# Kernel tuning notes

Measured on AMD Instinct MI355X. Metric: run time of the kernel, lower is better.

Reference implementation:

```python
import jax, jax.numpy as jnp
import numpy as np

B, S, E, H, V, O = 64, 512, 128, 1024, 128, 128


def setup_inputs() -> dict:
    key = jax.random.key(0)
    ks = jax.random.split(key, 16)
    nrm = lambda k, shp, s=0.05: s * jax.random.normal(k, shp, dtype=jnp.float32)
    return {
        "inputs": jax.random.randint(ks[0], (B, S), 0, V),
        "carry": jnp.zeros((B, H), dtype=jnp.float32),
        "embedding": nrm(ks[1], (V, E), 0.1),
        # GRUCell params (flax convention: input denses 'ir','iz','in' have bias;
        # hidden denses 'hr','hz' no bias; 'hn' has bias)
        "Wir": nrm(ks[2], (E, H)), "bir": jnp.zeros((H,), jnp.float32),
        "Whr": nrm(ks[3], (H, H)),
        "Wiz": nrm(ks[4], (E, H)), "biz": jnp.zeros((H,), jnp.float32),
        "Whz": nrm(ks[5], (H, H)),
        "Win": nrm(ks[6], (E, H)), "bin_": jnp.zeros((H,), jnp.float32),
        "Whn": nrm(ks[7], (H, H)), "bhn": jnp.zeros((H,), jnp.float32),
        "Wh": nrm(ks[8], (H, H)), "bh": jnp.zeros((H,), jnp.float32),
        "Wo": nrm(ks[9], (H, O)), "bo": jnp.zeros((O,), jnp.float32),
    }


def reference(inputs, carry, embedding, Wir, bir, Whr, Wiz, biz, Whz,
              Win, bin_, Whn, bhn, Wh, bh, Wo, bo):
    # Embedding lookup: [B, S, E]
    embed = jnp.take(embedding, inputs, axis=0)

    # GRU scan over time (axis=1 of embed)
    def step(h, x):  # h: [B,H], x: [B,E]
        r = jax.nn.sigmoid(x @ Wir + bir + h @ Whr)
        z = jax.nn.sigmoid(x @ Wiz + biz + h @ Whz)
        n = jnp.tanh(x @ Win + bin_ + r * (h @ Whn + bhn))
        h_new = (1.0 - z) * n + z * h
        return h_new, h_new

    xs = jnp.swapaxes(embed, 0, 1)  # [S, B, E]
    carry_out, ys = jax.lax.scan(step, carry, xs)  # ys: [S, B, H]
    outputs = jnp.swapaxes(ys, 0, 1).reshape(-1, H)  # [B*S, H]

    hidden = outputs @ Wh + bh            # Dense hidden_size
    logits = hidden @ Wo + bo             # Dense output_size -> [B*S, O]
    return (carry_out, logits)
```

## Files before the change

### kernel.cpp

```cpp
#include <hip/hip_runtime.h>
#include <hip/hip_cooperative_groups.h>
#include <math.h>

namespace cg = cooperative_groups;

#define Bp 64
#define Sp 512
#define Ep 128
#define Hp 1024
#define Vp 128
#define Op 128
#define BH (Bp * Hp)

typedef short s8v __attribute__((ext_vector_type(8)));
typedef float f4v __attribute__((ext_vector_type(4)));

#define WS_XV    0
#define WS_WHI   (WS_XV + Vp*3*Hp)
#define WS_WLO   (WS_WHI + (3*Hp*Hp)/2)
#define WS_YSH   (WS_WLO + (3*Hp*Hp)/2)
#define WS_HLOP  (WS_YSH + ((size_t)(Sp+1)*BH)/2)
#define WS_WHBH  (WS_HLOP + (2*BH)/2)
#define WS_WHBL  (WS_WHBH + (Hp*Hp)/2)
#define WS_WOBH  (WS_WHBL + (Hp*Hp)/2)
#define WS_WOBL  (WS_WOBH + (Op*Hp)/2)
#define WS_BAR   (WS_WOBL + (Op*Hp)/2)
#define WS_FLOATS (WS_BAR + 4*256)

__device__ __forceinline__ unsigned short f2bf(float x) {
  union { float f; unsigned u; } v; v.f = x;
  unsigned r = v.u + 0x7fffu + ((v.u >> 16) & 1u);
  return (unsigned short)(r >> 16);
}
__device__ __forceinline__ float bf2f(unsigned short h) {
  union { unsigned u; float f; } v; v.u = ((unsigned)h) << 16;
  return v.f;
}

__device__ __forceinline__ s8v ald16(const unsigned short* p) {
  union { unsigned long long q[2]; s8v v; } u;
  const unsigned long long* qp = (const unsigned long long*)p;
  u.q[0] = __hip_atomic_load(qp,     __ATOMIC_RELAXED, __HIP_MEMORY_SCOPE_AGENT);
  u.q[1] = __hip_atomic_load(qp + 1, __ATOMIC_RELAXED, __HIP_MEMORY_SCOPE_AGENT);
  return u.v;
}
__device__ __forceinline__ void ast8(unsigned short* p, unsigned long long v) {
  __hip_atomic_store((unsigned long long*)p, v, __ATOMIC_RELAXED, __HIP_MEMORY_SCOPE_AGENT);
}

__global__ __launch_bounds__(256) void xv_kernel(
    const float* __restrict__ emb,
    const float* __restrict__ Wir, const float* __restrict__ bir,
    const float* __restrict__ Wiz, const float* __restrict__ biz,
    const float* __restrict__ Win, const float* __restrict__ bin_,
    float* __restrict__ XV) {
  int n = blockIdx.x * 256 + threadIdx.x;
  int v = blockIdx.y;
  int g = n >> 10;
  int j = n & (Hp - 1);
  const float* W = (g == 0) ? Wir : ((g == 1) ? Wiz : Win);
  const float* bias = (g == 0) ? bir : ((g == 1) ? biz : bin_);
  float acc = bias[j];
  const float* ev = emb + (size_t)v * Ep;
  for (int e = 0; e < Ep; ++e) acc += ev[e] * W[(size_t)e * Hp + j];
  XV[(size_t)v * (3 * Hp) + n] = acc;
}

__global__ void wpack_kernel(const float* __restrict__ Whr,
                             const float* __restrict__ Whz,
                             const float* __restrict__ Whn,
                             unsigned short* __restrict__ Whi,
                             unsigned short* __restrict__ Wlo) {
  __shared__ float tile[32][33];
  int g = blockIdx.z;
  const float* src = (g == 0) ? Whr : ((g == 1) ? Whz : Whn);
  int kb = blockIdx.x * 32;
  int jb32 = blockIdx.y * 32;
  int tx = threadIdx.x, ty = threadIdx.y;
  #pragma unroll
  for (int i = 0; i < 4; ++i)
    tile[ty + 8 * i][tx] = src[(size_t)(kb + ty + 8 * i) * Hp + (jb32 + tx)];
  __syncthreads();
  #pragma unroll
  for (int i = 0; i < 4; ++i) {
    int jl = ty + 8 * i;
    int j = jb32 + jl;
    int dstRow = ((j >> 4) * 3 + g) * 16 + (j & 15);
    float w = tile[tx][jl];
    unsigned short hi = f2bf(w);
    Whi[(size_t)dstRow * Hp + kb + tx] = hi;
    Wlo[(size_t)dstRow * Hp + kb + tx] = f2bf(w - bf2f(hi));
  }
}

__global__ void tsplit_kernel(const float* __restrict__ src, int K, int N,
                              unsigned short* __restrict__ dhi,
                              unsigned short* __restrict__ dlo) {
  __shared__ float tile[32][33];
  int kb = blockIdx.x * 32, nb = blockIdx.y * 32;
  int tx = threadIdx.x, ty = threadIdx.y;
  #pragma unroll
  for (int i = 0; i < 4; ++i)
    tile[ty + 8 * i][tx] = src[(size_t)(kb + ty + 8 * i) * N + nb + tx];
  __syncthreads();
  #pragma unroll
  for (int i = 0; i < 4; ++i) {
    int nl = ty + 8 * i;
    float w = tile[tx][nl];
    unsigned short hi = f2bf(w);
    dhi[(size_t)(nb + nl) * K + kb + tx] = hi;
    dlo[(size_t)(nb + nl) * K + kb + tx] = f2bf(w - bf2f(hi));
  }
}

__global__ void h0_kernel(const float* __restrict__ carry,
                          unsigned short* __restrict__ ysH,
                          unsigned short* __restrict__ hloP,
                          unsigned* __restrict__ bar) {
  int i = blockIdx.x * 256 + threadIdx.x;
  float h = carry[i];
  unsigned short hi = f2bf(h);
  ysH[i] = hi;
  hloP[i] = f2bf(h - bf2f(hi));
  if (i < 4 * 256) bar[i] = 0u;
}

__global__ __launch_bounds__(256, 1) void gru_scan(
    const float* __restrict__ carry,
    unsigned short* ysH,
    const unsigned short* __restrict__ Whi,
    const unsigned short* __restrict__ Wlo,
    const float* __restrict__ XV,
    const int* __restrict__ toks,
    const float* __restrict__ bhn,
    unsigned short* hloP,
    unsigned* bar) {
  __shared__ float part[3 * 4 * 64 * 4];
  __shared__ unsigned short hst[2][16][16];

  const int tid = threadIdx.x;
  const int wv = tid >> 6, lane = tid & 63;
  const int mb = blockIdx.x >> 6, jb = blockIdx.x & 63;
  const int col = lane & 15, kq = lane >> 4;

  unsigned* ctr = bar + mb * 256;

  const int kbase = wv * 256 + kq * 8;
  const unsigned short* bhp[3];
  const unsigned short* blp[3];
  #pragma unroll
  for (int g = 0; g < 3; ++g) {
    const size_t rowoff = ((size_t)(jb * 3 + g) * 16 + col) * Hp + kbase;
    bhp[g] = Whi + rowoff;
    blp[g] = Wlo + rowoff;
  }

  const int erow = tid >> 4, ecol = tid & 15;
  const int eb = mb * 16 + erow;
  const int ej = jb * 16 + ecol;
  const int elane = (erow >> 2) * 16 + ecol;
  const int er = erow & 3;
  const float bhnv = bhn[ej];

  const size_t aBase = (size_t)(mb * 16 + col) * Hp + kbase;
  const size_t eOff = (size_t)eb * Hp + ej;

  float holdR = carry[eOff];
  int tok0 = toks[eb * Sp + 0];
  const float* xvp0 = XV + (size_t)tok0 * (3 * Hp) + ej;
  float xr = xvp0[0], xz = xvp0[Hp], xn = xvp0[2 * Hp];

  const int splane = tid >> 6;
  const int srow = (tid >> 2) & 15;
  const int squad = tid & 3;
  const size_t sOff = (size_t)(mb * 16 + srow) * Hp + jb * 16 + squad * 4;

  for (int t = 0; t < Sp; ++t) {
    const unsigned short* hhiR = ysH + (size_t)t * BH;
    const unsigned short* hloR = hloP + (size_t)(t & 1) * BH;
    unsigned short* hhiW = ysH + (size_t)(t + 1) * BH;
    unsigned short* hloW = hloP + (size_t)((t + 1) & 1) * BH;

    s8v ah[8], al[8];
    #pragma unroll
    for (int c = 0; c < 8; ++c) {
      ah[c] = ald16(hhiR + aBase + (size_t)c * 32);
      al[c] = ald16(hloR + aBase + (size_t)c * 32);
    }

    float xrN, xzN, xnN;
    {
      int tN = (t + 1 < Sp) ? (t + 1) : t;
      int tokN = toks[eb * Sp + tN];
      const float* xvpN = XV + (size_t)tokN * (3 * Hp) + ej;
      xrN = xvpN[0];
      xzN = xvpN[Hp];
      xnN = xvpN[2 * Hp];
    }

    f4v ar = {0.f, 0.f, 0.f, 0.f}, az = {0.f, 0.f, 0.f, 0.f}, an = {0.f, 0.f, 0.f, 0.f};
    #pragma unroll
    for (int c = 0; c < 8; ++c) {
      s8v b0 = *(const s8v*)(bhp[0] + c * 32);
      s8v b1 = *(const s8v*)(bhp[1] + c * 32);
      s8v b2 = *(const s8v*)(bhp[2] + c * 32);
      s8v l0 = *(const s8v*)(blp[0] + c * 32);
      s8v l1 = *(const s8v*)(blp[1] + c * 32);
      s8v l2 = *(const s8v*)(blp[2] + c * 32);
      ar = __builtin_amdgcn_mfma_f32_16x16x32_bf16(ah[c], b0, ar, 0, 0, 0);
      az = __builtin_amdgcn_mfma_f32_16x16x32_bf16(ah[c], b1, az, 0, 0, 0);
      an = __builtin_amdgcn_mfma_f32_16x16x32_bf16(ah[c], b2, an, 0, 0, 0);
      ar = __builtin_amdgcn_mfma_f32_16x16x32_bf16(al[c], b0, ar, 0, 0, 0);
      az = __builtin_amdgcn_mfma_f32_16x16x32_bf16(al[c], b1, az, 0, 0, 0);
      an = __builtin_amdgcn_mfma_f32_16x16x32_bf16(al[c], b2, an, 0, 0, 0);
      ar = __builtin_amdgcn_mfma_f32_16x16x32_bf16(ah[c], l0, ar, 0, 0, 0);
      az = __builtin_amdgcn_mfma_f32_16x16x32_bf16(ah[c], l1, az, 0, 0, 0);
      an = __builtin_amdgcn_mfma_f32_16x16x32_bf16(ah[c], l2, an, 0, 0, 0);
    }

    *(f4v*)&part[((0 * 4 + wv) * 64 + lane) * 4] = ar;
    *(f4v*)&part[((1 * 4 + wv) * 64 + lane) * 4] = az;
    *(f4v*)&part[((2 * 4 + wv) * 64 + lane) * 4] = an;
    __syncthreads();

    float sr = 0.f, sz = 0.f, sn = 0.f;
    #pragma unroll
    for (int w = 0; w < 4; ++w) {
      sr += part[((0 * 4 + w) * 64 + elane) * 4 + er];
      sz += part[((1 * 4 + w) * 64 + elane) * 4 + er];
      sn += part[((2 * 4 + w) * 64 + elane) * 4 + er];
    }

    float rg = 1.f / (1.f + expf(-(sr + xr)));
    float zg = 1.f / (1.f + expf(-(sz + xz)));
    float ng = tanhf(xn + rg * (sn + bhnv));
    float hnew = (1.f - zg) * ng + zg * holdR;

    unsigned short hi16 = f2bf(hnew);
    hst[0][erow][ecol] = hi16;
    hst[1][erow][ecol] = f2bf(hnew - bf2f(hi16));

    holdR = hnew;
    xr = xrN; xz = xzN; xn = xnN;

    __syncthreads();
    if (tid < 128) {
      unsigned long long v = *(const unsigned long long*)&hst[splane][srow][squad * 4];
      ast8((splane ? hloW : hhiW) + sOff, v);
    }

    __threadfence_block();
    __syncthreads();
    if (tid == 0) {
      __hip_atomic_fetch_add(ctr, 1u, __ATOMIC_RELAXED, __HIP_MEMORY_SCOPE_AGENT);
      unsigned target = 64u * (unsigned)(t + 1);
      while (__hip_atomic_load(ctr, __ATOMIC_RELAXED, __HIP_MEMORY_SCOPE_AGENT) < target)
        __builtin_amdgcn_s_sleep(2);
    }
    __syncthreads();
  }
}

__global__ __launch_bounds__(256, 1) void dense_kernel(
    const unsigned short* __restrict__ ysH,
    const unsigned short* __restrict__ WhbH, const unsigned short* __restrict__ WhbL,
    const float* __restrict__ bh,
    const unsigned short* __restrict__ WobH, const unsigned short* __restrict__ WobL,
    const float* __restrict__ bo,
    float* __restrict__ out) {
  __shared__ unsigned short aHi[32 * 16 * 4 * 8];
  __shared__ unsigned short hidBf[32 * 16 * 4 * 8];

  const int tid = threadIdx.x;
  const int wv = tid >> 6, lane = tid & 63;
  const int col = lane & 15, kq = lane >> 4;
  const int r0 = blockIdx.x * 16;
  const int bq = r0 / Sp, s0 = r0 % Sp;

  for (int i = tid; i < 16 * 128; i += 256) {
    int m = i >> 7, c8 = i & 127;
    int kc = c8 >> 2, kqi = c8 & 3;
    const uint4* src = (const uint4*)(ysH + ((size_t)(s0 + m + 1) * Bp + bq) * Hp) + c8;
    *(uint4*)&aHi[((kc * 16 + m) * 4 + kqi) * 8] = *src;
  }
  __syncthreads();

  f4v acc[16];
  #pragma unroll
  for (int nt = 0; nt < 16; ++nt) acc[nt] = (f4v){0.f, 0.f, 0.f, 0.f};
  for (int kc = 0; kc < 32; ++kc) {
    s8v a = *(const s8v*)&aHi[(kc * 64 + col * 4 + kq) * 8];
    const size_t koff = (size_t)kc * 32 + kq * 8;
    #pragma unroll
    for (int nt = 0; nt < 16; ++nt) {
      int n = wv * 256 + nt * 16 + col;
      s8v bHi = *(const s8v*)(WhbH + (size_t)n * Hp + koff);
      s8v bLo = *(const s8v*)(WhbL + (size_t)n * Hp + koff);
      acc[nt] = __builtin_amdgcn_mfma_f32_16x16x32_bf16(a, bHi, acc[nt], 0, 0, 0);
      acc[nt] = __builtin_amdgcn_mfma_f32_16x16x32_bf16(a, bLo, acc[nt], 0, 0, 0);
    }
  }
  #pragma unroll
  for (int nt = 0; nt < 16; ++nt) {
    int n = wv * 256 + nt * 16 + col;
    float bias = bh[n];
    int kc = n >> 5, kqi = (n >> 3) & 3, ii = n & 7;
    #pragma unroll
    for (int r = 0; r < 4; ++r) {
      int m = kq * 4 + r;
      hidBf[((kc * 16 + m) * 4 + kqi) * 8 + ii] = f2bf(acc[nt][r] + bias);
    }
  }
  __syncthreads();

  f4v lacc[2];
  lacc[0] = (f4v){0.f, 0.f, 0.f, 0.f};
  lacc[1] = (f4v){0.f, 0.f, 0.f, 0.f};
  for (int kc = 0; kc < 32; ++kc) {
    s8v a = *(const s8v*)&hidBf[(kc * 64 + col * 4 + kq) * 8];
    const size_t koff = (size_t)kc * 32 + kq * 8;
    #pragma unroll
    for (int ot = 0; ot < 2; ++ot) {
      int o = (wv * 2 + ot) * 16 + col;
      s8v bHi = *(const s8v*)(WobH + (size_t)o * Hp + koff);
      s8v bLo = *(const s8v*)(WobL + (size_t)o * Hp + koff);
      lacc[ot] = __builtin_amdgcn_mfma_f32_16x16x32_bf16(a, bHi, lacc[ot], 0, 0, 0);
      lacc[ot] = __builtin_amdgcn_mfma_f32_16x16x32_bf16(a, bLo, lacc[ot], 0, 0, 0);
    }
  }
  float* lo = out + (size_t)Bp * Hp;
  #pragma unroll
  for (int ot = 0; ot < 2; ++ot) {
    int o = (wv * 2 + ot) * 16 + col;
    float bias = bo[o];
    #pragma unroll
    for (int r = 0; r < 4; ++r) {
      int m = kq * 4 + r;
      lo[(size_t)(r0 + m) * Op + o] = lacc[ot][r] + bias;
    }
  }
}

__global__ void carry_kernel(const unsigned short* __restrict__ ysH,
                             const unsigned short* __restrict__ hloP,
                             float* __restrict__ out) {
  int i = blockIdx.x * 256 + threadIdx.x;
  out[i] = bf2f(ysH[(size_t)Sp * BH + i]) + bf2f(hloP[(size_t)(Sp & 1) * BH + i]);
}

extern "C" void kernel_launch(void* const* d_in, const int* in_sizes, int n_in,
                              void* d_out, int out_size, void* d_ws, size_t ws_size,
                              hipStream_t stream) {
  const int*   toks = (const int*)  d_in[0];
  const float* carry= (const float*)d_in[1];
  const float* emb  = (const float*)d_in[2];
  const float* Wir  = (const float*)d_in[3];
  const float* bir  = (const float*)d_in[4];
  const float* Whr  = (const float*)d_in[5];
  const float* Wiz  = (const float*)d_in[6];
  const float* biz  = (const float*)d_in[7];
  const float* Whz  = (const float*)d_in[8];
  const float* Win  = (const float*)d_in[9];
  const float* bin_ = (const float*)d_in[10];
  const float* Whn  = (const float*)d_in[11];
  const float* bhn  = (const float*)d_in[12];
  const float* Wh   = (const float*)d_in[13];
  const float* bh   = (const float*)d_in[14];
  const float* Wo   = (const float*)d_in[15];
  const float* bo   = (const float*)d_in[16];
  float* out = (float*)d_out;

  if (ws_size < WS_FLOATS * sizeof(float)) return;

  float* ws = (float*)d_ws;
  float* XV = ws + WS_XV;
  unsigned short* WhiP = (unsigned short*)(ws + WS_WHI);
  unsigned short* WloP = (unsigned short*)(ws + WS_WLO);
  unsigned short* ysH  = (unsigned short*)(ws + WS_YSH);
  unsigned short* hloP = (unsigned short*)(ws + WS_HLOP);
  unsigned short* WhbH = (unsigned short*)(ws + WS_WHBH);
  unsigned short* WhbL = (unsigned short*)(ws + WS_WHBL);
  unsigned short* WobH = (unsigned short*)(ws + WS_WOBH);
  unsigned short* WobL = (unsigned short*)(ws + WS_WOBL);
  unsigned* bar = (unsigned*)(ws + WS_BAR);

  xv_kernel<<<dim3(12, Vp), 256, 0, stream>>>(emb, Wir, bir, Wiz, biz, Win, bin_, XV);
  wpack_kernel<<<dim3(Hp / 32, Hp / 32, 3), dim3(32, 8), 0, stream>>>(Whr, Whz, Whn, WhiP, WloP);
  tsplit_kernel<<<dim3(Hp / 32, Hp / 32), dim3(32, 8), 0, stream>>>(Wh, Hp, Hp, WhbH, WhbL);
  tsplit_kernel<<<dim3(Hp / 32, Op / 32), dim3(32, 8), 0, stream>>>(Wo, Hp, Op, WobH, WobL);
  h0_kernel<<<BH / 256, 256, 0, stream>>>(carry, ysH, hloP, bar);

  {
    void* args[] = {(void*)&carry, (void*)&ysH, (void*)&WhiP, (void*)&WloP,
                    (void*)&XV, (void*)&toks, (void*)&bhn,
                    (void*)&hloP, (void*)&bar};
    hipLaunchCooperativeKernel((const void*)gru_scan, dim3(256), dim3(256),
                               args, 0, stream);
  }

  carry_kernel<<<BH / 256, 256, 0, stream>>>(ysH, hloP, out);
  dense_kernel<<<(Bp * Sp) / 16, 256, 0, stream>>>(ysH, WhbH, WhbL, bh, WobH, WobL, bo, out);
}
```

Baseline: 4.516 ms.

## Replace per-group counter barrier with per-block flags and two batch groups per block

The scan kernel now launches 128 blocks instead of 256. Each block handles one hidden-column tile for two batch groups in turn. The atomic counter barrier that every block spun on is replaced by per-(batch group, column block) step flags, so a block waits only until the 64 producers of the group it is about to read have published. The goal is to cut barrier latency and let one group's compute overlap with the other group's wait. The cost is that each block does twice the sequential MFMA work per step and there is half as much parallelism.

```diff
diff --git a/kernel.cpp b/kernel.cpp
--- a/kernel.cpp
+++ b/kernel.cpp
@@ -24,8 +24,8 @@
 #define WS_WHBL  (WS_WHBH + (Hp*Hp)/2)
 #define WS_WOBH  (WS_WHBL + (Hp*Hp)/2)
 #define WS_WOBL  (WS_WOBH + (Op*Hp)/2)
-#define WS_BAR   (WS_WOBL + (Op*Hp)/2)
-#define WS_FLOATS (WS_BAR + 4*256)
+#define WS_FLG   (WS_WOBL + (Op*Hp)/2)
+#define WS_FLOATS (WS_FLG + 1024)
 
 __device__ __forceinline__ unsigned short f2bf(float x) {
   union { float f; unsigned u; } v; v.f = x;
@@ -116,13 +116,13 @@
 __global__ void h0_kernel(const float* __restrict__ carry,
                           unsigned short* __restrict__ ysH,
                           unsigned short* __restrict__ hloP,
-                          unsigned* __restrict__ bar) {
+                          unsigned* __restrict__ flg) {
   int i = blockIdx.x * 256 + threadIdx.x;
   float h = carry[i];
   unsigned short hi = f2bf(h);
   ysH[i] = hi;
   hloP[i] = f2bf(h - bf2f(hi));
-  if (i < 4 * 256) bar[i] = 0u;
+  if (i < 1024) flg[i] = 0u;
 }
 
 __global__ __launch_bounds__(256, 1) void gru_scan(
@@ -134,16 +134,14 @@
     const int* __restrict__ toks,
     const float* __restrict__ bhn,
     unsigned short* hloP,
-    unsigned* bar) {
+    unsigned* flg) {
   __shared__ float part[3 * 4 * 64 * 4];
   __shared__ unsigned short hst[2][16][16];
 
   const int tid = threadIdx.x;
   const int wv = tid >> 6, lane = tid & 63;
-  const int mb = blockIdx.x >> 6, jb = blockIdx.x & 63;
+  const int jb = blockIdx.x >> 1, mp = blockIdx.x & 1;
   const int col = lane & 15, kq = lane >> 4;
-
-  unsigned* ctr = bar + mb * 256;
 
   const int kbase = wv * 256 + kq * 8;
   const unsigned short* bhp[3];
@@ -156,24 +154,32 @@
   }
 
   const int erow = tid >> 4, ecol = tid & 15;
-  const int eb = mb * 16 + erow;
   const int ej = jb * 16 + ecol;
   const int elane = (erow >> 2) * 16 + ecol;
   const int er = erow & 3;
   const float bhnv = bhn[ej];
 
-  const size_t aBase = (size_t)(mb * 16 + col) * Hp + kbase;
-  const size_t eOff = (size_t)eb * Hp + ej;
-
-  float holdR = carry[eOff];
-  int tok0 = toks[eb * Sp + 0];
-  const float* xvp0 = XV + (size_t)tok0 * (3 * Hp) + ej;
-  float xr = xvp0[0], xz = xvp0[Hp], xn = xvp0[2 * Hp];
-
   const int splane = tid >> 6;
   const int srow = (tid >> 2) & 15;
   const int squad = tid & 3;
-  const size_t sOff = (size_t)(mb * 16 + srow) * Hp + jb * 16 + squad * 4;
+
+  int mbA[2];
+  int ebA[2];
+  size_t aBase[2], eOff[2], sOff[2];
+  float holdR[2], xr[2], xz[2], xn[2];
+  #pragma unroll
+  for (int i = 0; i < 2; ++i) {
+    int mb = 2 * mp + i;
+    mbA[i] = mb;
+    ebA[i] = mb * 16 + erow;
+    aBase[i] = (size_t)(mb * 16 + col) * Hp + kbase;
+    eOff[i] = (size_t)ebA[i] * Hp + ej;
+    sOff[i] = (size_t)(mb * 16 + srow) * Hp + jb * 16 + squad * 4;
+    holdR[i] = carry[eOff[i]];
+    int tok0 = toks[ebA[i] * Sp + 0];
+    const float* xvp0 = XV + (size_t)tok0 * (3 * Hp) + ej;
+    xr[i] = xvp0[0]; xz[i] = xvp0[Hp]; xn[i] = xvp0[2 * Hp];
+  }
 
   for (int t = 0; t < Sp; ++t) {
     const unsigned short* hhiR = ysH + (size_t)t * BH;
@@ -181,83 +187,92 @@
     unsigned short* hhiW = ysH + (size_t)(t + 1) * BH;
     unsigned short* hloW = hloP + (size_t)((t + 1) & 1) * BH;
 
-    s8v ah[8], al[8];
-    #pragma unroll
-    for (int c = 0; c < 8; ++c) {
-      ah[c] = ald16(hhiR + aBase + (size_t)c * 32);
-      al[c] = ald16(hloR + aBase + (size_t)c * 32);
+    for (int i = 0; i < 2; ++i) {
+      const int mb = mbA[i];
+
+      if (t > 0) {
+        const unsigned* fp = flg + mb * 64 + lane;
+        while (true) {
+          unsigned f = __hip_atomic_load(fp, __ATOMIC_RELAXED, __HIP_MEMORY_SCOPE_AGENT);
+          if (__all((int)(f >= (unsigned)t))) break;
+          __builtin_amdgcn_s_sleep(1);
+        }
+      }
+
+      s8v ah[8], al[8];
+      #pragma unroll
+      for (int c = 0; c < 8; ++c) {
+        ah[c] = ald16(hhiR + aBase[i] + (size_t)c * 32);
+        al[c] = ald16(hloR + aBase[i] + (size_t)c * 32);
+      }
+
+      float xrN, xzN, xnN;
+      {
+        int tN = (t + 1 < Sp) ? (t + 1) : t;
+        int tokN = toks[ebA[i] * Sp + tN];
+        const float* xvpN = XV + (size_t)tokN * (3 * Hp) + ej;
+        xrN = xvpN[0];
+        xzN = xvpN[Hp];
+        xnN = xvpN[2 * Hp];
+      }
+
+      f4v ar = {0.f, 0.f, 0.f, 0.f}, az = {0.f, 0.f, 0.f, 0.f}, an = {0.f, 0.f, 0.f, 0.f};
+      #pragma unroll
+      for (int c = 0; c < 8; ++c) {
+        s8v b0 = *(const s8v*)(bhp[0] + c * 32);
+        s8v b1 = *(const s8v*)(bhp[1] + c * 32);
+        s8v b2 = *(const s8v*)(bhp[2] + c * 32);
+        s8v l0 = *(const s8v*)(blp[0] + c * 32);
+        s8v l1 = *(const s8v*)(blp[1] + c * 32);
+        s8v l2 = *(const s8v*)(blp[2] + c * 32);
+        ar = __builtin_amdgcn_mfma_f32_16x16x32_bf16(ah[c], b0, ar, 0, 0, 0);
+        az = __builtin_amdgcn_mfma_f32_16x16x32_bf16(ah[c], b1, az, 0, 0, 0);
+        an = __builtin_amdgcn_mfma_f32_16x16x32_bf16(ah[c], b2, an, 0, 0, 0);
+        ar = __builtin_amdgcn_mfma_f32_16x16x32_bf16(al[c], b0, ar, 0, 0, 0);
+        az = __builtin_amdgcn_mfma_f32_16x16x32_bf16(al[c], b1, az, 0, 0, 0);
+        an = __builtin_amdgcn_mfma_f32_16x16x32_bf16(al[c], b2, an, 0, 0, 0);
+        ar = __builtin_amdgcn_mfma_f32_16x16x32_bf16(ah[c], l0, ar, 0, 0, 0);
+        az = __builtin_amdgcn_mfma_f32_16x16x32_bf16(ah[c], l1, az, 0, 0, 0);
+        an = __builtin_amdgcn_mfma_f32_16x16x32_bf16(ah[c], l2, an, 0, 0, 0);
+      }
+
+      *(f4v*)&part[((0 * 4 + wv) * 64 + lane) * 4] = ar;
+      *(f4v*)&part[((1 * 4 + wv) * 64 + lane) * 4] = az;
+      *(f4v*)&part[((2 * 4 + wv) * 64 + lane) * 4] = an;
+      __syncthreads();
+
+      float sr = 0.f, sz = 0.f, sn = 0.f;
+      #pragma unroll
+      for (int w = 0; w < 4; ++w) {
+        sr += part[((0 * 4 + w) * 64 + elane) * 4 + er];
+        sz += part[((1 * 4 + w) * 64 + elane) * 4 + er];
+        sn += part[((2 * 4 + w) * 64 + elane) * 4 + er];
+      }
+
+      float rg = 1.f / (1.f + expf(-(sr + xr[i])));
+      float zg = 1.f / (1.f + expf(-(sz + xz[i])));
+      float ng = tanhf(xn[i] + rg * (sn + bhnv));
+      float hnew = (1.f - zg) * ng + zg * holdR[i];
+
+      unsigned short hi16 = f2bf(hnew);
+      hst[0][erow][ecol] = hi16;
+      hst[1][erow][ecol] = f2bf(hnew - bf2f(hi16));
+
+      holdR[i] = hnew;
+      xr[i] = xrN; xz[i] = xzN; xn[i] = xnN;
+
+      __syncthreads();
+      if (tid < 128) {
+        unsigned long long v = *(const unsigned long long*)&hst[splane][srow][squad * 4];
+        ast8((splane ? hloW : hhiW) + sOff[i], v);
+      }
+
+      __threadfence_block();
+      __syncthreads();
+      if (tid == 0)
+        __hip_atomic_store(flg + mb * 64 + jb, (unsigned)(t + 1),
+                           __ATOMIC_RELAXED, __HIP_MEMORY_SCOPE_AGENT);
     }
-
-    float xrN, xzN, xnN;
-    {
-      int tN = (t + 1 < Sp) ? (t + 1) : t;
-      int tokN = toks[eb * Sp + tN];
-      const float* xvpN = XV + (size_t)tokN * (3 * Hp) + ej;
-      xrN = xvpN[0];
-      xzN = xvpN[Hp];
-      xnN = xvpN[2 * Hp];
-    }
-
-    f4v ar = {0.f, 0.f, 0.f, 0.f}, az = {0.f, 0.f, 0.f, 0.f}, an = {0.f, 0.f, 0.f, 0.f};
-    #pragma unroll
-    for (int c = 0; c < 8; ++c) {
-      s8v b0 = *(const s8v*)(bhp[0] + c * 32);
-      s8v b1 = *(const s8v*)(bhp[1] + c * 32);
-      s8v b2 = *(const s8v*)(bhp[2] + c * 32);
-      s8v l0 = *(const s8v*)(blp[0] + c * 32);
-      s8v l1 = *(const s8v*)(blp[1] + c * 32);
-      s8v l2 = *(const s8v*)(blp[2] + c * 32);
-      ar = __builtin_amdgcn_mfma_f32_16x16x32_bf16(ah[c], b0, ar, 0, 0, 0);
-      az = __builtin_amdgcn_mfma_f32_16x16x32_bf16(ah[c], b1, az, 0, 0, 0);
-      an = __builtin_amdgcn_mfma_f32_16x16x32_bf16(ah[c], b2, an, 0, 0, 0);
-      ar = __builtin_amdgcn_mfma_f32_16x16x32_bf16(al[c], b0, ar, 0, 0, 0);
-      az = __builtin_amdgcn_mfma_f32_16x16x32_bf16(al[c], b1, az, 0, 0, 0);
-      an = __builtin_amdgcn_mfma_f32_16x16x32_bf16(al[c], b2, an, 0, 0, 0);
-      ar = __builtin_amdgcn_mfma_f32_16x16x32_bf16(ah[c], l0, ar, 0, 0, 0);
-      az = __builtin_amdgcn_mfma_f32_16x16x32_bf16(ah[c], l1, az, 0, 0, 0);
-      an = __builtin_amdgcn_mfma_f32_16x16x32_bf16(ah[c], l2, an, 0, 0, 0);
-    }
-
-    *(f4v*)&part[((0 * 4 + wv) * 64 + lane) * 4] = ar;
-    *(f4v*)&part[((1 * 4 + wv) * 64 + lane) * 4] = az;
-    *(f4v*)&part[((2 * 4 + wv) * 64 + lane) * 4] = an;
-    __syncthreads();
-
-    float sr = 0.f, sz = 0.f, sn = 0.f;
-    #pragma unroll
-    for (int w = 0; w < 4; ++w) {
-      sr += part[((0 * 4 + w) * 64 + elane) * 4 + er];
-      sz += part[((1 * 4 + w) * 64 + elane) * 4 + er];
-      sn += part[((2 * 4 + w) * 64 + elane) * 4 + er];
-    }
-
-    float rg = 1.f / (1.f + expf(-(sr + xr)));
-    float zg = 1.f / (1.f + expf(-(sz + xz)));
-    float ng = tanhf(xn + rg * (sn + bhnv));
-    float hnew = (1.f - zg) * ng + zg * holdR;
-
-    unsigned short hi16 = f2bf(hnew);
-    hst[0][erow][ecol] = hi16;
-    hst[1][erow][ecol] = f2bf(hnew - bf2f(hi16));
-
-    holdR = hnew;
-    xr = xrN; xz = xzN; xn = xnN;
-
-    __syncthreads();
-    if (tid < 128) {
-      unsigned long long v = *(const unsigned long long*)&hst[splane][srow][squad * 4];
-      ast8((splane ? hloW : hhiW) + sOff, v);
-    }
-
-    __threadfence_block();
-    __syncthreads();
-    if (tid == 0) {
-      __hip_atomic_fetch_add(ctr, 1u, __ATOMIC_RELAXED, __HIP_MEMORY_SCOPE_AGENT);
-      unsigned target = 64u * (unsigned)(t + 1);
-      while (__hip_atomic_load(ctr, __ATOMIC_RELAXED, __HIP_MEMORY_SCOPE_AGENT) < target)
-        __builtin_amdgcn_s_sleep(2);
-    }
-    __syncthreads();
   }
 }
 
@@ -382,19 +397,19 @@
   unsigned short* WhbL = (unsigned short*)(ws + WS_WHBL);
   unsigned short* WobH = (unsigned short*)(ws + WS_WOBH);
   unsigned short* WobL = (unsigned short*)(ws + WS_WOBL);
-  unsigned* bar = (unsigned*)(ws + WS_BAR);
+  unsigned* flg = (unsigned*)(ws + WS_FLG);
 
   xv_kernel<<<dim3(12, Vp), 256, 0, stream>>>(emb, Wir, bir, Wiz, biz, Win, bin_, XV);
   wpack_kernel<<<dim3(Hp / 32, Hp / 32, 3), dim3(32, 8), 0, stream>>>(Whr, Whz, Whn, WhiP, WloP);
   tsplit_kernel<<<dim3(Hp / 32, Hp / 32), dim3(32, 8), 0, stream>>>(Wh, Hp, Hp, WhbH, WhbL);
   tsplit_kernel<<<dim3(Hp / 32, Op / 32), dim3(32, 8), 0, stream>>>(Wo, Hp, Op, WobH, WobL);
-  h0_kernel<<<BH / 256, 256, 0, stream>>>(carry, ysH, hloP, bar);
+  h0_kernel<<<BH / 256, 256, 0, stream>>>(carry, ysH, hloP, flg);
 
   {
     void* args[] = {(void*)&carry, (void*)&ysH, (void*)&WhiP, (void*)&WloP,
                     (void*)&XV, (void*)&toks, (void*)&bhn,
-                    (void*)&hloP, (void*)&bar};
-    hipLaunchCooperativeKernel((const void*)gru_scan, dim3(256), dim3(256),
+                    (void*)&hloP, (void*)&flg};
+    hipLaunchCooperativeKernel((const void*)gru_scan, dim3(128), dim3(256),
                                args, 0, stream);
   }
 
```

Measured after the change: 7.289 ms. 1.61x slower.

## Replace per-step counter barrier with tagged hidden-state records polled by consumers

Applied to the files above, without the earlier changes.

Removes the per-timestep atomic counter barrier in the GRU scan. Each 64-bit record now packs hi/lo bf16 pairs with a 2-bit step tag stolen from the low mantissa bits of the lo part, and consumers spin until all their loaded records carry the expected tag. This eliminates the fetch-add, the spin on a shared counter and two block-wide syncs per step, and it also reorders the block-to-tile mapping. The cost is slightly reduced precision in the lo correction term and a launch that is no longer cooperative, so forward progress assumes all 256 blocks are co-resident.

```diff
diff --git a/kernel.cpp b/kernel.cpp
--- a/kernel.cpp
+++ b/kernel.cpp
@@ -1,8 +1,5 @@
 #include <hip/hip_runtime.h>
-#include <hip/hip_cooperative_groups.h>
 #include <math.h>
-
-namespace cg = cooperative_groups;
 
 #define Bp 64
 #define Sp 512
@@ -19,13 +16,12 @@
 #define WS_WHI   (WS_XV + Vp*3*Hp)
 #define WS_WLO   (WS_WHI + (3*Hp*Hp)/2)
 #define WS_YSH   (WS_WLO + (3*Hp*Hp)/2)
-#define WS_HLOP  (WS_YSH + ((size_t)(Sp+1)*BH)/2)
-#define WS_WHBH  (WS_HLOP + (2*BH)/2)
+#define WS_HX    (WS_YSH + ((size_t)(Sp+1)*BH)/2)
+#define WS_WHBH  (WS_HX + 2*(BH/2)*2)
 #define WS_WHBL  (WS_WHBH + (Hp*Hp)/2)
 #define WS_WOBH  (WS_WHBL + (Hp*Hp)/2)
 #define WS_WOBL  (WS_WOBH + (Op*Hp)/2)
-#define WS_BAR   (WS_WOBL + (Op*Hp)/2)
-#define WS_FLOATS (WS_BAR + 4*256)
+#define WS_FLOATS (WS_WOBL + (Op*Hp)/2)
 
 __device__ __forceinline__ unsigned short f2bf(float x) {
   union { float f; unsigned u; } v; v.f = x;
@@ -35,17 +31,6 @@
 __device__ __forceinline__ float bf2f(unsigned short h) {
   union { unsigned u; float f; } v; v.u = ((unsigned)h) << 16;
   return v.f;
-}
-
-__device__ __forceinline__ s8v ald16(const unsigned short* p) {
-  union { unsigned long long q[2]; s8v v; } u;
-  const unsigned long long* qp = (const unsigned long long*)p;
-  u.q[0] = __hip_atomic_load(qp,     __ATOMIC_RELAXED, __HIP_MEMORY_SCOPE_AGENT);
-  u.q[1] = __hip_atomic_load(qp + 1, __ATOMIC_RELAXED, __HIP_MEMORY_SCOPE_AGENT);
-  return u.v;
-}
-__device__ __forceinline__ void ast8(unsigned short* p, unsigned long long v) {
-  __hip_atomic_store((unsigned long long*)p, v, __ATOMIC_RELAXED, __HIP_MEMORY_SCOPE_AGENT);
 }
 
 __global__ __launch_bounds__(256) void xv_kernel(
@@ -114,36 +99,35 @@
 }
 
 __global__ void h0_kernel(const float* __restrict__ carry,
-                          unsigned short* __restrict__ ysH,
-                          unsigned short* __restrict__ hloP,
-                          unsigned* __restrict__ bar) {
+                          unsigned long long* __restrict__ hx) {
   int i = blockIdx.x * 256 + threadIdx.x;
-  float h = carry[i];
-  unsigned short hi = f2bf(h);
-  ysH[i] = hi;
-  hloP[i] = f2bf(h - bf2f(hi));
-  if (i < 4 * 256) bar[i] = 0u;
+  int b = i >> 9, jp = i & 511;
+  float f0 = carry[(size_t)b * Hp + 2 * jp];
+  float f1 = carry[(size_t)b * Hp + 2 * jp + 1];
+  unsigned long long h0 = f2bf(f0);
+  unsigned long long l0 = (f2bf(f0 - bf2f((unsigned short)h0)) & 0xFFFCu) | 3u;
+  unsigned long long h1 = f2bf(f1);
+  unsigned long long l1 = (f2bf(f1 - bf2f((unsigned short)h1)) & 0xFFFCu) | 3u;
+  unsigned long long rec = h0 | (l0 << 16) | (h1 << 32) | (l1 << 48);
+  __hip_atomic_store(hx + (BH / 2) + i, rec, __ATOMIC_RELAXED, __HIP_MEMORY_SCOPE_AGENT);
 }
 
 __global__ __launch_bounds__(256, 1) void gru_scan(
     const float* __restrict__ carry,
-    unsigned short* ysH,
+    unsigned short* __restrict__ ysH,
     const unsigned short* __restrict__ Whi,
     const unsigned short* __restrict__ Wlo,
     const float* __restrict__ XV,
     const int* __restrict__ toks,
     const float* __restrict__ bhn,
-    unsigned short* hloP,
-    unsigned* bar) {
+    unsigned long long* hx) {
   __shared__ float part[3 * 4 * 64 * 4];
   __shared__ unsigned short hst[2][16][16];
 
   const int tid = threadIdx.x;
   const int wv = tid >> 6, lane = tid & 63;
-  const int mb = blockIdx.x >> 6, jb = blockIdx.x & 63;
+  const int mb = blockIdx.x & 3, jb = blockIdx.x >> 2;
   const int col = lane & 15, kq = lane >> 4;
-
-  unsigned* ctr = bar + mb * 256;
 
   const int kbase = wv * 256 + kq * 8;
   const unsigned short* bhp[3];
@@ -162,30 +146,43 @@
   const int er = erow & 3;
   const float bhnv = bhn[ej];
 
-  const size_t aBase = (size_t)(mb * 16 + col) * Hp + kbase;
   const size_t eOff = (size_t)eb * Hp + ej;
+  const size_t rBase = (size_t)(mb * 16 + col) * 512 + wv * 128 + kq * 4;
 
   float holdR = carry[eOff];
   int tok0 = toks[eb * Sp + 0];
   const float* xvp0 = XV + (size_t)tok0 * (3 * Hp) + ej;
   float xr = xvp0[0], xz = xvp0[Hp], xn = xvp0[2 * Hp];
 
-  const int splane = tid >> 6;
-  const int srow = (tid >> 2) & 15;
-  const int squad = tid & 3;
-  const size_t sOff = (size_t)(mb * 16 + srow) * Hp + jb * 16 + squad * 4;
-
   for (int t = 0; t < Sp; ++t) {
-    const unsigned short* hhiR = ysH + (size_t)t * BH;
-    const unsigned short* hloR = hloP + (size_t)(t & 1) * BH;
-    unsigned short* hhiW = ysH + (size_t)(t + 1) * BH;
-    unsigned short* hloW = hloP + (size_t)((t + 1) & 1) * BH;
+    const unsigned long long* hxR = hx + (size_t)((t + 1) & 1) * (BH / 2);
+    unsigned long long* hxW = hx + (size_t)(t & 1) * (BH / 2);
+    const unsigned tagR = (unsigned)((t + 3) & 3);
+    const unsigned long long Mv = (0x3ULL << 16) | (0x3ULL << 48);
+    const unsigned long long Ev = ((unsigned long long)tagR << 16) |
+                                  ((unsigned long long)tagR << 48);
 
     s8v ah[8], al[8];
-    #pragma unroll
-    for (int c = 0; c < 8; ++c) {
-      ah[c] = ald16(hhiR + aBase + (size_t)c * 32);
-      al[c] = ald16(hloR + aBase + (size_t)c * 32);
+    while (true) {
+      int ok = 1;
+      #pragma unroll
+      for (int c = 0; c < 8; ++c) {
+        union { unsigned u[4]; s8v v; } H, L;
+        #pragma unroll
+        for (int rr = 0; rr < 4; ++rr) {
+          unsigned long long q = __hip_atomic_load(hxR + rBase + c * 16 + rr,
+                                     __ATOMIC_RELAXED, __HIP_MEMORY_SCOPE_AGENT);
+          ok &= ((q & Mv) == Ev) ? 1 : 0;
+          unsigned lo32 = (unsigned)q;
+          unsigned hi32 = (unsigned)(q >> 32);
+          H.u[rr] = __builtin_amdgcn_perm(hi32, lo32, 0x05040100u);
+          L.u[rr] = __builtin_amdgcn_perm(hi32, lo32, 0x07060302u);
+        }
+        ah[c] = H.v;
+        al[c] = L.v;
+      }
+      if (__all(ok)) break;
+      __builtin_amdgcn_s_sleep(1);
     }
 
     float xrN, xzN, xnN;
@@ -244,20 +241,24 @@
     xr = xrN; xz = xzN; xn = xnN;
 
     __syncthreads();
+
+    const unsigned tagW = (unsigned)(t & 3);
     if (tid < 128) {
-      unsigned long long v = *(const unsigned long long*)&hst[splane][srow][squad * 4];
-      ast8((splane ? hloW : hhiW) + sOff, v);
-    }
-
-    __threadfence_block();
-    __syncthreads();
-    if (tid == 0) {
-      __hip_atomic_fetch_add(ctr, 1u, __ATOMIC_RELAXED, __HIP_MEMORY_SCOPE_AGENT);
-      unsigned target = 64u * (unsigned)(t + 1);
-      while (__hip_atomic_load(ctr, __ATOMIC_RELAXED, __HIP_MEMORY_SCOPE_AGENT) < target)
-        __builtin_amdgcn_s_sleep(2);
-    }
-    __syncthreads();
+      int r = tid >> 3, p = tid & 7;
+      unsigned long long h0 = hst[0][r][2 * p];
+      unsigned long long l0 = (hst[1][r][2 * p] & 0xFFFCu) | tagW;
+      unsigned long long h1 = hst[0][r][2 * p + 1];
+      unsigned long long l1 = (hst[1][r][2 * p + 1] & 0xFFFCu) | tagW;
+      unsigned long long rec = h0 | (l0 << 16) | (h1 << 32) | (l1 << 48);
+      __hip_atomic_store(hxW + (size_t)(mb * 16 + r) * 512 + jb * 8 + p, rec,
+                         __ATOMIC_RELAXED, __HIP_MEMORY_SCOPE_AGENT);
+    } else {
+      int t2 = tid - 128;
+      int r = t2 >> 3, p = t2 & 7;
+      unsigned dw = (unsigned)hst[0][r][2 * p] | ((unsigned)hst[0][r][2 * p + 1] << 16);
+      __builtin_nontemporal_store(dw,
+          (unsigned*)(ysH + (size_t)(t + 1) * BH + (size_t)(mb * 16 + r) * Hp + jb * 16 + 2 * p));
+    }
   }
 }
 
@@ -342,10 +343,13 @@
 }
 
 __global__ void carry_kernel(const unsigned short* __restrict__ ysH,
-                             const unsigned short* __restrict__ hloP,
+                             const unsigned long long* __restrict__ hx,
                              float* __restrict__ out) {
   int i = blockIdx.x * 256 + threadIdx.x;
-  out[i] = bf2f(ysH[(size_t)Sp * BH + i]) + bf2f(hloP[(size_t)(Sp & 1) * BH + i]);
+  int b = i >> 10, j = i & 1023;
+  unsigned long long rec = hx[(BH / 2) + (size_t)b * 512 + (j >> 1)];
+  unsigned short lo16 = (unsigned short)((rec >> (16 + 32 * (j & 1))) & 0xFFFCu);
+  out[i] = bf2f(ysH[(size_t)Sp * BH + i]) + bf2f(lo16);
 }
 
 extern "C" void kernel_launch(void* const* d_in, const int* in_sizes, int n_in,
@@ -377,27 +381,21 @@
   unsigned short* WhiP = (unsigned short*)(ws + WS_WHI);
   unsigned short* WloP = (unsigned short*)(ws + WS_WLO);
   unsigned short* ysH  = (unsigned short*)(ws + WS_YSH);
-  unsigned short* hloP = (unsigned short*)(ws + WS_HLOP);
+  unsigned long long* hx = (unsigned long long*)(ws + WS_HX);
   unsigned short* WhbH = (unsigned short*)(ws + WS_WHBH);
   unsigned short* WhbL = (unsigned short*)(ws + WS_WHBL);
   unsigned short* WobH = (unsigned short*)(ws + WS_WOBH);
   unsigned short* WobL = (unsigned short*)(ws + WS_WOBL);
-  unsigned* bar = (unsigned*)(ws + WS_BAR);
 
   xv_kernel<<<dim3(12, Vp), 256, 0, stream>>>(emb, Wir, bir, Wiz, biz, Win, bin_, XV);
   wpack_kernel<<<dim3(Hp / 32, Hp / 32, 3), dim3(32, 8), 0, stream>>>(Whr, Whz, Whn, WhiP, WloP);
   tsplit_kernel<<<dim3(Hp / 32, Hp / 32), dim3(32, 8), 0, stream>>>(Wh, Hp, Hp, WhbH, WhbL);
   tsplit_kernel<<<dim3(Hp / 32, Op / 32), dim3(32, 8), 0, stream>>>(Wo, Hp, Op, WobH, WobL);
-  h0_kernel<<<BH / 256, 256, 0, stream>>>(carry, ysH, hloP, bar);
-
-  {
-    void* args[] = {(void*)&carry, (void*)&ysH, (void*)&WhiP, (void*)&WloP,
-                    (void*)&XV, (void*)&toks, (void*)&bhn,
-                    (void*)&hloP, (void*)&bar};
-    hipLaunchCooperativeKernel((const void*)gru_scan, dim3(256), dim3(256),
-                               args, 0, stream);
-  }
-
-  carry_kernel<<<BH / 256, 256, 0, stream>>>(ysH, hloP, out);
+  h0_kernel<<<(BH / 2) / 256, 256, 0, stream>>>(carry, hx);
+
+  gru_scan<<<dim3(256), dim3(256), 0, stream>>>(carry, ysH, WhiP, WloP,
+                                                XV, toks, bhn, hx);
+
+  carry_kernel<<<BH / 256, 256, 0, stream>>>(ysH, hx, out);
   dense_kernel<<<(Bp * Sp) / 16, 256, 0, stream>>>(ysH, WhbH, WhbL, bh, WobH, WobL, bo, out);
 }
```

Result: slower. 5.049 ms (+11.8%).

## Replace counter barrier with per-block progress flags polled by a wavefront

Applied to the files above, without the earlier changes.

Each block in the GRU scan no longer joins a shared atomic counter barrier at the end of every step. It publishes its step number in its own flag slot. Before the next step, one wavefront-wide load polls the 64 flags of its batch group until all have reached the current step. This removes the fetch-add contention, the single-thread spin and one block-wide sync per step. The change also swaps the block index mapping, switches to a plain (non-cooperative) launch and adds restrict qualifiers. It relies on relaxed atomics for ordering, and on all 256 blocks being co-resident without a cooperative-launch guarantee.

```diff
diff --git a/kernel.cpp b/kernel.cpp
--- a/kernel.cpp
+++ b/kernel.cpp
@@ -1,8 +1,5 @@
 #include <hip/hip_runtime.h>
-#include <hip/hip_cooperative_groups.h>
 #include <math.h>
-
-namespace cg = cooperative_groups;
 
 #define Bp 64
 #define Sp 512
@@ -24,8 +21,8 @@
 #define WS_WHBL  (WS_WHBH + (Hp*Hp)/2)
 #define WS_WOBH  (WS_WHBL + (Hp*Hp)/2)
 #define WS_WOBL  (WS_WOBH + (Op*Hp)/2)
-#define WS_BAR   (WS_WOBL + (Op*Hp)/2)
-#define WS_FLOATS (WS_BAR + 4*256)
+#define WS_FLG   (WS_WOBL + (Op*Hp)/2)
+#define WS_FLOATS (WS_FLG + 256)
 
 __device__ __forceinline__ unsigned short f2bf(float x) {
   union { float f; unsigned u; } v; v.f = x;
@@ -116,34 +113,32 @@
 __global__ void h0_kernel(const float* __restrict__ carry,
                           unsigned short* __restrict__ ysH,
                           unsigned short* __restrict__ hloP,
-                          unsigned* __restrict__ bar) {
+                          unsigned* __restrict__ flg) {
   int i = blockIdx.x * 256 + threadIdx.x;
   float h = carry[i];
   unsigned short hi = f2bf(h);
   ysH[i] = hi;
   hloP[i] = f2bf(h - bf2f(hi));
-  if (i < 4 * 256) bar[i] = 0u;
+  if (i < 256) flg[i] = 0u;
 }
 
 __global__ __launch_bounds__(256, 1) void gru_scan(
     const float* __restrict__ carry,
-    unsigned short* ysH,
+    unsigned short* __restrict__ ysH,
     const unsigned short* __restrict__ Whi,
     const unsigned short* __restrict__ Wlo,
     const float* __restrict__ XV,
     const int* __restrict__ toks,
     const float* __restrict__ bhn,
-    unsigned short* hloP,
-    unsigned* bar) {
+    unsigned short* __restrict__ hloP,
+    unsigned* __restrict__ flg) {
   __shared__ float part[3 * 4 * 64 * 4];
   __shared__ unsigned short hst[2][16][16];
 
   const int tid = threadIdx.x;
   const int wv = tid >> 6, lane = tid & 63;
-  const int mb = blockIdx.x >> 6, jb = blockIdx.x & 63;
+  const int mb = blockIdx.x & 3, jb = blockIdx.x >> 2;
   const int col = lane & 15, kq = lane >> 4;
-
-  unsigned* ctr = bar + mb * 256;
 
   const int kbase = wv * 256 + kq * 8;
   const unsigned short* bhp[3];
@@ -175,11 +170,21 @@
   const int squad = tid & 3;
   const size_t sOff = (size_t)(mb * 16 + srow) * Hp + jb * 16 + squad * 4;
 
+  const unsigned* fp = flg + mb * 64 + lane;
+
   for (int t = 0; t < Sp; ++t) {
     const unsigned short* hhiR = ysH + (size_t)t * BH;
     const unsigned short* hloR = hloP + (size_t)(t & 1) * BH;
     unsigned short* hhiW = ysH + (size_t)(t + 1) * BH;
     unsigned short* hloW = hloP + (size_t)((t + 1) & 1) * BH;
+
+    if (t > 0) {
+      while (true) {
+        unsigned f = __hip_atomic_load(fp, __ATOMIC_RELAXED, __HIP_MEMORY_SCOPE_AGENT);
+        if (__all((int)(f >= (unsigned)t))) break;
+        __builtin_amdgcn_s_sleep(1);
+      }
+    }
 
     s8v ah[8], al[8];
     #pragma unroll
@@ -251,13 +256,9 @@
 
     __threadfence_block();
     __syncthreads();
-    if (tid == 0) {
-      __hip_atomic_fetch_add(ctr, 1u, __ATOMIC_RELAXED, __HIP_MEMORY_SCOPE_AGENT);
-      unsigned target = 64u * (unsigned)(t + 1);
-      while (__hip_atomic_load(ctr, __ATOMIC_RELAXED, __HIP_MEMORY_SCOPE_AGENT) < target)
-        __builtin_amdgcn_s_sleep(2);
-    }
-    __syncthreads();
+    if (tid == 0)
+      __hip_atomic_store(flg + mb * 64 + jb, (unsigned)(t + 1),
+                         __ATOMIC_RELAXED, __HIP_MEMORY_SCOPE_AGENT);
   }
 }
 
@@ -345,7 +346,7 @@
                              const unsigned short* __restrict__ hloP,
                              float* __restrict__ out) {
   int i = blockIdx.x * 256 + threadIdx.x;
-  out[i] = bf2f(ysH[(size_t)Sp * BH + i]) + bf2f(hloP[(size_t)(Sp & 1) * BH + i]);
+  out[i] = bf2f(ysH[(size_t)Sp * BH + i]) + bf2f(hloP[i]);
 }
 
 extern "C" void kernel_launch(void* const* d_in, const int* in_sizes, int n_in,
@@ -382,21 +383,16 @@
   unsigned short* WhbL = (unsigned short*)(ws + WS_WHBL);
   unsigned short* WobH = (unsigned short*)(ws + WS_WOBH);
   unsigned short* WobL = (unsigned short*)(ws + WS_WOBL);
-  unsigned* bar = (unsigned*)(ws + WS_BAR);
+  unsigned* flg = (unsigned*)(ws + WS_FLG);
 
   xv_kernel<<<dim3(12, Vp), 256, 0, stream>>>(emb, Wir, bir, Wiz, biz, Win, bin_, XV);
   wpack_kernel<<<dim3(Hp / 32, Hp / 32, 3), dim3(32, 8), 0, stream>>>(Whr, Whz, Whn, WhiP, WloP);
   tsplit_kernel<<<dim3(Hp / 32, Hp / 32), dim3(32, 8), 0, stream>>>(Wh, Hp, Hp, WhbH, WhbL);
   tsplit_kernel<<<dim3(Hp / 32, Op / 32), dim3(32, 8), 0, stream>>>(Wo, Hp, Op, WobH, WobL);
-  h0_kernel<<<BH / 256, 256, 0, stream>>>(carry, ysH, hloP, bar);
-
-  {
-    void* args[] = {(void*)&carry, (void*)&ysH, (void*)&WhiP, (void*)&WloP,
-                    (void*)&XV, (void*)&toks, (void*)&bhn,
-                    (void*)&hloP, (void*)&bar};
-    hipLaunchCooperativeKernel((const void*)gru_scan, dim3(256), dim3(256),
-                               args, 0, stream);
-  }
+  h0_kernel<<<BH / 256, 256, 0, stream>>>(carry, ysH, hloP, flg);
+
+  gru_scan<<<dim3(256), dim3(256), 0, stream>>>(carry, ysH, WhiP, WloP,
+                                                XV, toks, bhn, hloP, flg);
 
   carry_kernel<<<BH / 256, 256, 0, stream>>>(ysH, hloP, out);
   dense_kernel<<<(Bp * Sp) / 16, 256, 0, stream>>>(ysH, WhbH, WhbL, bh, WobH, WobL, bo, out);
```

Result: slower. 4.849 ms (+7.4%).
